# Optimization experiments

Measured on AMD Instinct MI355X. Metric: run time of the kernel, lower is better.

The kernel has to match this reference:

```python
import jax, jax.numpy as jnp
import numpy as np

EMBED, HEADS, LEVELS, POINTS = 256, 8, 4, 4
SPATIAL_SHAPES = np.array([[128, 128], [64, 64], [32, 32], [16, 16]], dtype=np.int32)


def _grid_init_bias():
    # Faithful reproduction of the sampling_offsets bias init (per-head directional grid).
    thetas = np.arange(HEADS, dtype=np.float32) * (2.0 * np.pi / HEADS)
    g = np.stack([np.cos(thetas), np.sin(thetas)], -1)
    g = g / np.abs(g).max(-1, keepdims=True)
    g = np.tile(g.reshape(HEADS, 1, 1, 2), (1, LEVELS, POINTS, 1))
    for i in range(POINTS):
        g[:, :, i, :] *= i + 1
    return g.reshape(-1).astype(np.float32)


def setup_inputs() -> dict:
    key = jax.random.key(0)
    ks = jax.random.split(key, 8)
    bs = 2
    V = int((SPATIAL_SHAPES[:, 0] * SPATIAL_SHAPES[:, 1]).sum())  # 21760
    Q = V  # encoder self-attention
    C = EMBED
    n_off = HEADS * LEVELS * POINTS * 2
    n_attn = HEADS * LEVELS * POINTS
    inv_sqrt_c = 1.0 / np.sqrt(C)
    return {
        "query": jax.random.normal(ks[0], (bs, Q, C), jnp.float32),
        "value": jax.random.normal(ks[1], (bs, V, C), jnp.float32),
        "reference_points": jax.random.uniform(ks[2], (bs, Q, LEVELS, 2), jnp.float32),
        "spatial_shapes": SPATIAL_SHAPES,  # static int array
        # learned parameters (torch Linear stored as [in, out]: y = x @ W + b)
        "W_off": jax.random.normal(ks[3], (C, n_off), jnp.float32) * 0.01,
        "b_off": jnp.asarray(_grid_init_bias()),
        "W_attn": jax.random.normal(ks[4], (C, n_attn), jnp.float32) * 0.02,
        "b_attn": jnp.zeros((n_attn,), jnp.float32),
        "W_v": jax.random.normal(ks[5], (C, C), jnp.float32) * inv_sqrt_c,
        "b_v": jnp.zeros((C,), jnp.float32),
        "W_out": jax.random.normal(ks[6], (C, C), jnp.float32) * inv_sqrt_c,
        "b_out": jnp.zeros((C,), jnp.float32),
    }


def _ms_deform_attn(query, value, reference_points, shapes,
                    W_off, b_off, W_attn, b_attn, W_v, b_v, W_out, b_out):
    bs, Q, C = query.shape
    d = C // HEADS
    # value projection -> [bs, heads, V, d]
    val = (value @ W_v + b_v).reshape(bs, -1, HEADS, d).transpose(0, 2, 1, 3)
    # sampling offsets and attention weights from query
    off = (query @ W_off + b_off).reshape(bs, Q, HEADS, LEVELS, POINTS, 2)
    attn = jax.nn.softmax(
        (query @ W_attn + b_attn).reshape(bs, Q, HEADS, LEVELS * POINTS), axis=-1
    ).reshape(bs, Q, HEADS, LEVELS, POINTS)
    # offset normalizer is (W, H) per level
    norm = jnp.asarray(np.stack([shapes[:, 1], shapes[:, 0]], -1), jnp.float32)  # [L,2]
    loc = reference_points[:, :, None, :, None, :] + off / norm[None, None, None, :, None, :]

    out = jnp.zeros((bs, HEADS, Q, d), query.dtype)
    start = 0
    for l in range(LEVELS):
        H, W = int(shapes[l, 0]), int(shapes[l, 1])
        v_l = val[:, :, start:start + H * W]  # [bs, heads, H*W, d]
        start += H * W
        loc_l = loc[:, :, :, l]    # [bs, Q, heads, P, 2] in [0,1]
        attn_l = attn[:, :, :, l]  # [bs, Q, heads, P]
        # grid_sample(align_corners=False, padding_mode='zeros') semantics
        g = 2.0 * loc_l - 1.0
        x = (g[..., 0] + 1.0) * 0.5 * W - 0.5
        y = (g[..., 1] + 1.0) * 0.5 * H - 0.5
        x0 = jnp.floor(x)
        y0 = jnp.floor(y)
        for dx in (0, 1):
            for dy in (0, 1):
                xi = x0 + dx
                yi = y0 + dy
                w = (1.0 - jnp.abs(x - xi)) * (1.0 - jnp.abs(y - yi))
                valid = (xi >= 0) & (xi <= W - 1) & (yi >= 0) & (yi <= H - 1)
                w = jnp.where(valid, w, 0.0) * attn_l  # fused corner + attention weight
                idx = (jnp.clip(yi, 0, H - 1).astype(jnp.int32) * W
                       + jnp.clip(xi, 0, W - 1).astype(jnp.int32))  # [bs,Q,heads,P]
                idx_t = jnp.transpose(idx, (0, 2, 1, 3)).reshape(bs, HEADS, Q * POINTS)
                vals = jnp.take_along_axis(v_l, idx_t[..., None], axis=2)
                vals = vals.reshape(bs, HEADS, Q, POINTS, d)
                out = out + jnp.einsum('bhqpd,bqhp->bhqd', vals, w)
    out = out.transpose(0, 2, 1, 3).reshape(bs, Q, C)  # heads-major channel layout
    return out @ W_out + b_out


def reference(query, value, reference_points, spatial_shapes,
              W_off, b_off, W_attn, b_attn, W_v, b_v, W_out, b_out):
    shapes = np.asarray(spatial_shapes)  # static
    return _ms_deform_attn(query, value, reference_points, shapes,
                           W_off, b_off, W_attn, b_attn, W_v, b_v, W_out, b_out)
```

## Files before the change

kernel.cpp:

```cpp
#include <hip/hip_runtime.h>
#include <math.h>

#define QN 21760
#define MTOT 43520
#define SZBQC 11141120

typedef __attribute__((ext_vector_type(8))) short bf16x8;
typedef __attribute__((ext_vector_type(4))) float f32x4;

__device__ inline ushort f2bf(float f) {
  union { float f; uint u; } v; v.f = f;
  return (ushort)((v.u + 0x7FFFu + ((v.u >> 16) & 1u)) >> 16);
}
__device__ inline uint pk2(float lo, float hi) { return (uint)f2bf(lo) | ((uint)f2bf(hi) << 16); }

__device__ inline void g2l(const ushort* g, ushort* l) {
  __builtin_amdgcn_global_load_lds(
      (const __attribute__((address_space(1))) void*)g,
      (__attribute__((address_space(3))) void*)l, 16, 0, 0);
}

__global__ __launch_bounds__(256) void prep_weights(
    const float* __restrict__ Wv, const float* __restrict__ Wout,
    const float* __restrict__ Woff, const float* __restrict__ Wattn,
    const float* __restrict__ boff, const float* __restrict__ battn,
    ushort* __restrict__ wv_t, ushort* __restrict__ wout_t,
    ushort* __restrict__ wol_t, float* __restrict__ biasf) {
  int bidx = blockIdx.x, t = threadIdx.x;
  if (bidx < 256) {
    int idx = bidx * 256 + t; int n = idx >> 8, k = idx & 255;
    wv_t[idx] = f2bf(Wv[(size_t)k * 256 + n]);
  } else if (bidx < 512) {
    int idx = (bidx - 256) * 256 + t; int n = idx >> 8, k = idx & 255;
    wout_t[idx] = f2bf(Wout[(size_t)k * 256 + n]);
  } else {
    int idx = (bidx - 512) * 256 + t; int n = idx >> 8, k = idx & 255;
    float v = (n < 256) ? Woff[(size_t)k * 256 + n] : Wattn[(size_t)k * 128 + (n - 256)];
    wol_t[idx] = f2bf(v);
    if (idx < 384) biasf[idx] = (idx < 256) ? boff[idx] : battn[idx - 256];
  }
}


__global__ __launch_bounds__(256) void gemm_in(
    const float* __restrict__ value, const float* __restrict__ query,
    const ushort* __restrict__ Wv, const ushort* __restrict__ Wol,
    const float* __restrict__ bv, const float* __restrict__ bol,
    ushort* __restrict__ val_out, float* __restrict__ offlog) {
  __shared__ ushort As[2][4096];
  __shared__ ushort Bs[2][4096];
  const int t = threadIdx.x, wave = t >> 6, lane = t & 63;
  const int bx = blockIdx.y, bm = blockIdx.x * 128;
  const bool isVal = bx < 2;
  const float* A   = isVal ? value : query;
  const ushort* Bt = isVal ? (Wv + (size_t)bx * 128 * 256)
                           : (Wol + (size_t)(bx - 2) * 128 * 256);
  const int wm = (wave >> 1) * 64, wn = (wave & 1) * 64;
  const int l15 = lane & 15, l4 = lane >> 4;
  const int pc = l4 ^ ((l15 >> 1) & 3);

  const int srow = lane >> 2;
  const int sch  = (lane & 3) ^ ((lane >> 3) & 3);
  const ushort* Bg = Bt + (size_t)(32 * wave + srow) * 256 + sch * 8;
  ushort* lb[2] = { &Bs[0][(32 * wave) * 32], &Bs[1][(32 * wave) * 32] };

  f32x4 acc[4][4];
#pragma unroll
  for (int i = 0; i < 4; ++i)
#pragma unroll
    for (int j = 0; j < 4; ++j) acc[i][j] = (f32x4){0.f, 0.f, 0.f, 0.f};

  int arow[4], apart[4];
#pragma unroll
  for (int i = 0; i < 4; ++i) {
    int c = t + i * 256; arow[i] = c >> 3; apart[i] = c & 7;
  }

  {
    float4 pa[4];
#pragma unroll
    for (int i = 0; i < 4; ++i)
      pa[i] = *(const float4*)&A[(size_t)(bm + arow[i]) * 256 + apart[i] * 4];
    g2l(Bg, lb[0]); g2l(Bg + 16 * 256, lb[0] + 16 * 32);
#pragma unroll
    for (int i = 0; i < 4; ++i) {
      int pc16 = (apart[i] >> 1) ^ ((arow[i] >> 1) & 3);
      ushort4 hv = { f2bf(pa[i].x), f2bf(pa[i].y), f2bf(pa[i].z), f2bf(pa[i].w) };
      *(ushort4*)&As[0][arow[i] * 32 + pc16 * 8 + (apart[i] & 1) * 4] = hv;
    }
  }

  for (int k = 0; k < 8; ++k) {
    __syncthreads();
    const int cur = k & 1, nxt = cur ^ 1;
    float4 pa[4];
    if (k < 7) {
      int k1 = (k + 1) * 32;
#pragma unroll
      for (int i = 0; i < 4; ++i)
        pa[i] = *(const float4*)&A[(size_t)(bm + arow[i]) * 256 + k1 + apart[i] * 4];
      g2l(Bg + k1, lb[nxt]); g2l(Bg + 16 * 256 + k1, lb[nxt] + 16 * 32);
    }
    bf16x8 af[4], bfr[4];
#pragma unroll
    for (int mi = 0; mi < 4; ++mi)
      af[mi] = *(const bf16x8*)&As[cur][(wm + mi * 16 + l15) * 32 + pc * 8];
#pragma unroll
    for (int ni = 0; ni < 4; ++ni)
      bfr[ni] = *(const bf16x8*)&Bs[cur][(wn + ni * 16 + l15) * 32 + pc * 8];
#pragma unroll
    for (int mi = 0; mi < 4; ++mi)
#pragma unroll
      for (int ni = 0; ni < 4; ++ni)
        acc[mi][ni] = __builtin_amdgcn_mfma_f32_16x16x32_bf16(af[mi], bfr[ni], acc[mi][ni], 0, 0, 0);
    if (k < 7) {
#pragma unroll
      for (int i = 0; i < 4; ++i) {
        int pc16 = (apart[i] >> 1) ^ ((arow[i] >> 1) & 3);
        ushort4 hv = { f2bf(pa[i].x), f2bf(pa[i].y), f2bf(pa[i].z), f2bf(pa[i].w) };
        *(ushort4*)&As[nxt][arow[i] * 32 + pc16 * 8 + (apart[i] & 1) * 4] = hv;
      }
    }
  }

  if (isVal) {
    _Float16* vo = (_Float16*)val_out;
#pragma unroll
    for (int mi = 0; mi < 4; ++mi)
#pragma unroll
      for (int ni = 0; ni < 4; ++ni) {
        int col = bx * 128 + wn + ni * 16 + l15;
        float bb = bv[col];
        int hh = col >> 5, c = col & 31;
#pragma unroll
        for (int r = 0; r < 4; ++r) {
          int row = bm + wm + mi * 16 + l4 * 4 + r;
          int b = (row >= QN) ? 1 : 0;
          int vpos = row - b * QN;
          vo[((size_t)(b * 8 + hh) * QN + vpos) * 32 + c] = (_Float16)(acc[mi][ni][r] + bb);
        }
      }
  } else {
#pragma unroll
    for (int mi = 0; mi < 4; ++mi)
#pragma unroll
      for (int ni = 0; ni < 4; ++ni) {
        int col = (bx - 2) * 128 + wn + ni * 16 + l15;
        float bb = bol[col];
#pragma unroll
        for (int r = 0; r < 4; ++r) {
          int row = bm + wm + mi * 16 + l4 * 4 + r;
          offlog[(size_t)row * 384 + col] = acc[mi][ni][r] + bb;
        }
      }
  }
}

__global__ __launch_bounds__(256) void gemm_out(
    const ushort* __restrict__ A, const ushort* __restrict__ Bt,
    const float* __restrict__ bias, float* __restrict__ C) {
  __shared__ ushort As[2][4096];
  __shared__ ushort Bs[2][4096];
  const int t = threadIdx.x, wave = t >> 6, lane = t & 63;
  const int bm = blockIdx.x * 128, bn = blockIdx.y * 128;
  const int wm = (wave >> 1) * 64, wn = (wave & 1) * 64;
  const int l15 = lane & 15, l4 = lane >> 4;
  const int pc = l4 ^ ((l15 >> 1) & 3);

  const int srow = lane >> 2;
  const int sch  = (lane & 3) ^ ((lane >> 3) & 3);
  const ushort* Ag = A + (size_t)(bm + 32 * wave + srow) * 256 + sch * 8;
  const ushort* Bg = Bt + (size_t)(bn + 32 * wave + srow) * 256 + sch * 8;
  ushort* la[2] = { &As[0][(32 * wave) * 32], &As[1][(32 * wave) * 32] };
  ushort* lb[2] = { &Bs[0][(32 * wave) * 32], &Bs[1][(32 * wave) * 32] };

  f32x4 acc[4][4];
#pragma unroll
  for (int i = 0; i < 4; ++i)
#pragma unroll
    for (int j = 0; j < 4; ++j) acc[i][j] = (f32x4){0.f, 0.f, 0.f, 0.f};

  g2l(Ag, la[0]); g2l(Ag + 16 * 256, la[0] + 16 * 32);
  g2l(Bg, lb[0]); g2l(Bg + 16 * 256, lb[0] + 16 * 32);

  for (int k = 0; k < 8; ++k) {
    __syncthreads();
    const int cur = k & 1, nxt = cur ^ 1;
    if (k < 7) {
      int k1 = (k + 1) * 32;
      g2l(Ag + k1, la[nxt]); g2l(Ag + 16 * 256 + k1, la[nxt] + 16 * 32);
      g2l(Bg + k1, lb[nxt]); g2l(Bg + 16 * 256 + k1, lb[nxt] + 16 * 32);
    }
    bf16x8 af[4], bfr[4];
#pragma unroll
    for (int mi = 0; mi < 4; ++mi)
      af[mi] = *(const bf16x8*)&As[cur][(wm + mi * 16 + l15) * 32 + pc * 8];
#pragma unroll
    for (int ni = 0; ni < 4; ++ni)
      bfr[ni] = *(const bf16x8*)&Bs[cur][(wn + ni * 16 + l15) * 32 + pc * 8];
#pragma unroll
    for (int mi = 0; mi < 4; ++mi)
#pragma unroll
      for (int ni = 0; ni < 4; ++ni)
        acc[mi][ni] = __builtin_amdgcn_mfma_f32_16x16x32_bf16(af[mi], bfr[ni], acc[mi][ni], 0, 0, 0);
  }

#pragma unroll
  for (int mi = 0; mi < 4; ++mi)
#pragma unroll
    for (int ni = 0; ni < 4; ++ni) {
      int col = bn + wn + ni * 16 + l15;
      float bb = bias[col];
#pragma unroll
      for (int r = 0; r < 4; ++r) {
        int row = bm + wm + mi * 16 + l4 * 4 + r;
        C[(size_t)row * 256 + col] = acc[mi][ni][r] + bb;
      }
    }
}

__device__ inline void fmah(float* a, uint4 u, float wv) {
  union { uint4 u; _Float16 h[8]; } c; c.u = u;
#pragma unroll
  for (int i = 0; i < 8; ++i) a[i] = fmaf((float)c.h[i], wv, a[i]);
}

__global__ __launch_bounds__(256) void msda_sample(
    const ushort* __restrict__ val, const float* __restrict__ offlog,
    const float* __restrict__ ref, ushort* __restrict__ interm) {
  const int lsz[4]    = {128, 64, 32, 16};
  const int lstart[4] = {0, 16384, 20480, 21504};

  int h   = blockIdx.x & 7;
  int z   = blockIdx.x >> 3;
  int sub = threadIdx.x & 3;
  int bq  = z * 64 + (threadIdx.x >> 2);
  int b   = (bq >= QN) ? 1 : 0;

  const float* lgp = offlog + (size_t)bq * 384 + 256 + h * 16;
  float w[16];
  {
    float4 a0 = *(const float4*)(lgp);
    float4 a1 = *(const float4*)(lgp + 4);
    float4 a2 = *(const float4*)(lgp + 8);
    float4 a3 = *(const float4*)(lgp + 12);
    w[0]=a0.x; w[1]=a0.y; w[2]=a0.z; w[3]=a0.w;
    w[4]=a1.x; w[5]=a1.y; w[6]=a1.z; w[7]=a1.w;
    w[8]=a2.x; w[9]=a2.y; w[10]=a2.z; w[11]=a2.w;
    w[12]=a3.x; w[13]=a3.y; w[14]=a3.z; w[15]=a3.w;
  }
  float m = -1e30f;
#pragma unroll
  for (int s = 0; s < 16; ++s) m = fmaxf(m, w[s]);
  float sum = 0.f;
#pragma unroll
  for (int s = 0; s < 16; ++s) { w[s] = __expf(w[s] - m); sum += w[s]; }
  float inv = 1.f / sum;

  const float* offp = offlog + (size_t)bq * 384 + h * 32;
  const float* refp = ref + (size_t)bq * 8;
  const ushort* vb  = val + ((size_t)(b * 8 + h) * QN) * 32 + sub * 8;

  float acc[8];
#pragma unroll
  for (int i = 0; i < 8; ++i) acc[i] = 0.f;

#pragma unroll
  for (int l = 0; l < 4; ++l) {
    float4 o0 = *(const float4*)(offp + l * 8);
    float4 o1 = *(const float4*)(offp + l * 8 + 4);
    float ox[4] = { o0.x, o0.z, o1.x, o1.z };
    float oy[4] = { o0.y, o0.w, o1.y, o1.w };
    const int   W = lsz[l];
    const float fW = (float)W;
    const int   base = lstart[l];
    const float rx = refp[l * 2 + 0], ry = refp[l * 2 + 1];
#pragma unroll
    for (int p = 0; p < 4; ++p) {
      float x = rx * fW + ox[p] - 0.5f;
      float y = ry * fW + oy[p] - 0.5f;
      float x0f = floorf(x), y0f = floorf(y);
      int   x0 = (int)x0f,   y0 = (int)y0f;
      float fx = x - x0f,    fy = y - y0f;
      float a = w[l * 4 + p] * inv;
      const ushort* r0 = vb + (size_t)(base + y0 * W + x0) * 32;
      const ushort* r1 = r0 + (size_t)W * 32;

      if (x0 >= 0 && y0 >= 0 && x0 + 1 < W && y0 + 1 < W) {
        uint4 u00 = *(const uint4*)r0;
        uint4 u10 = *(const uint4*)(r0 + 32);
        uint4 u01 = *(const uint4*)r1;
        uint4 u11 = *(const uint4*)(r1 + 32);
        float w00 = (1.f - fx) * (1.f - fy) * a;
        float w10 = fx * (1.f - fy) * a;
        float w01 = (1.f - fx) * fy * a;
        float w11 = fx * fy * a;
        fmah(acc, u00, w00); fmah(acc, u10, w10);
        fmah(acc, u01, w01); fmah(acc, u11, w11);
      } else {
        float wx0 = (x0 >= 0 && x0 < W) ? (1.f - fx) : 0.f;
        float wx1 = (x0 + 1 >= 0 && x0 + 1 < W) ? fx : 0.f;
        float wy0 = (y0 >= 0 && y0 < W) ? (1.f - fy) : 0.f;
        float wy1 = (y0 + 1 >= 0 && y0 + 1 < W) ? fy : 0.f;
        float w00 = wx0 * wy0 * a, w10 = wx1 * wy0 * a;
        float w01 = wx0 * wy1 * a, w11 = wx1 * wy1 * a;
        if (w00 != 0.f) { uint4 u = *(const uint4*)r0;        fmah(acc, u, w00); }
        if (w10 != 0.f) { uint4 u = *(const uint4*)(r0 + 32); fmah(acc, u, w10); }
        if (w01 != 0.f) { uint4 u = *(const uint4*)r1;        fmah(acc, u, w01); }
        if (w11 != 0.f) { uint4 u = *(const uint4*)(r1 + 32); fmah(acc, u, w11); }
      }
    }
  }

  uint4 o;
  o.x = pk2(acc[0], acc[1]); o.y = pk2(acc[2], acc[3]);
  o.z = pk2(acc[4], acc[5]); o.w = pk2(acc[6], acc[7]);
  *(uint4*)(interm + (size_t)bq * 256 + h * 32 + sub * 8) = o;
}

extern "C" void kernel_launch(void* const* d_in, const int* in_sizes, int n_in,
                              void* d_out, int out_size, void* d_ws, size_t ws_size,
                              hipStream_t stream) {
  const float* query = (const float*)d_in[0];
  const float* value = (const float*)d_in[1];
  const float* ref   = (const float*)d_in[2];
  const float* W_off  = (const float*)d_in[4];
  const float* b_off  = (const float*)d_in[5];
  const float* W_attn = (const float*)d_in[6];
  const float* b_attn = (const float*)d_in[7];
  const float* W_v    = (const float*)d_in[8];
  const float* b_v    = (const float*)d_in[9];
  const float* W_out  = (const float*)d_in[10];
  const float* b_out  = (const float*)d_in[11];
  float* out = (float*)d_out;

  char* wsb = (char*)d_ws;
  ushort* ws_wv     = (ushort*)(wsb + 0);
  ushort* ws_wol    = (ushort*)(wsb + 131072);
  ushort* ws_wout   = (ushort*)(wsb + 327680);
  float*  ws_biasf  = (float*)(wsb + 458752);
  ushort* ws_val    = (ushort*)(wsb + 462848);
  ushort* ws_interm = (ushort*)(wsb + 22745088);
  float*  ws_offlog = (float*)(wsb + 45027328);
  size_t need = (size_t)45027328 + 66846720;
  if (ws_size < need) return;

  dim3 blk(256);
  prep_weights<<<dim3(896), blk, 0, stream>>>(W_v, W_out, W_off, W_attn, b_off, b_attn,
                                              ws_wv, ws_wout, ws_wol, ws_biasf);
  gemm_in<<<dim3(340, 5), blk, 0, stream>>>(value, query, ws_wv, ws_wol, b_v, ws_biasf,
                                            ws_val, ws_offlog);
  msda_sample<<<dim3(5440), blk, 0, stream>>>(ws_val, ws_offlog, ref, ws_interm);
  gemm_out<<<dim3(340, 2), blk, 0, stream>>>(ws_interm, ws_wout, b_out, out);
}
```

Measured before the change: 286.6 us.

## Keep full-K A tile resident in LDS and sweep all N panels per block

New measurement: 290.4 us. About the same (+1.3%).

```diff
diff --git a/kernel.cpp b/kernel.cpp
--- a/kernel.cpp
+++ b/kernel.cpp
@@ -3,7 +3,6 @@
 
 #define QN 21760
 #define MTOT 43520
-#define SZBQC 11141120
 
 typedef __attribute__((ext_vector_type(8))) short bf16x8;
 typedef __attribute__((ext_vector_type(4))) float f32x4;
@@ -42,181 +41,186 @@
 }
 
 
-__global__ __launch_bounds__(256) void gemm_in(
+__global__ __launch_bounds__(256) void gemm_in2(
     const float* __restrict__ value, const float* __restrict__ query,
     const ushort* __restrict__ Wv, const ushort* __restrict__ Wol,
     const float* __restrict__ bv, const float* __restrict__ bol,
     ushort* __restrict__ val_out, float* __restrict__ offlog) {
-  __shared__ ushort As[2][4096];
+  __shared__ ushort Ares[8 * 2048];
   __shared__ ushort Bs[2][4096];
   const int t = threadIdx.x, wave = t >> 6, lane = t & 63;
-  const int bx = blockIdx.y, bm = blockIdx.x * 128;
-  const bool isVal = bx < 2;
-  const float* A   = isVal ? value : query;
-  const ushort* Bt = isVal ? (Wv + (size_t)bx * 128 * 256)
-                           : (Wol + (size_t)(bx - 2) * 128 * 256);
-  const int wm = (wave >> 1) * 64, wn = (wave & 1) * 64;
+  const int bm = blockIdx.x * 64;
+  const bool isVal = (blockIdx.y == 0);
+  const float* A    = isVal ? value : query;
+  const ushort* Bt0 = isVal ? Wv : Wol;
+  const int np = isVal ? 2 : 3;
   const int l15 = lane & 15, l4 = lane >> 4;
   const int pc = l4 ^ ((l15 >> 1) & 3);
-
-  const int srow = lane >> 2;
-  const int sch  = (lane & 3) ^ ((lane >> 3) & 3);
-  const ushort* Bg = Bt + (size_t)(32 * wave + srow) * 256 + sch * 8;
+  const int wm = (wave >> 1) * 32, wn = (wave & 1) * 64;
+
+  const float4* Af4 = (const float4*)(A + (size_t)bm * 256);
+#pragma unroll
+  for (int i = 0; i < 16; ++i) {
+    int f = i * 256 + t;
+    int row = f >> 6, col4 = f & 63;
+    float4 v = Af4[f];
+    int k = col4 >> 3, part = col4 & 7;
+    int pc16 = (part >> 1) ^ ((row >> 1) & 3);
+    ushort4 hv = { f2bf(v.x), f2bf(v.y), f2bf(v.z), f2bf(v.w) };
+    *(ushort4*)&Ares[k * 2048 + row * 32 + pc16 * 8 + (part & 1) * 4] = hv;
+  }
+
+  const int srow = lane >> 2, sch = (lane & 3) ^ ((lane >> 3) & 3);
+  const int brow = 32 * wave + srow;
   ushort* lb[2] = { &Bs[0][(32 * wave) * 32], &Bs[1][(32 * wave) * 32] };
-
-  f32x4 acc[4][4];
-#pragma unroll
-  for (int i = 0; i < 4; ++i)
+  {
+    const ushort* Bg = Bt0 + (size_t)brow * 256 + sch * 8;
+    g2l(Bg, lb[0]); g2l(Bg + 16 * 256, lb[0] + 16 * 32);
+  }
+
+  f32x4 acc[2][4];
+#pragma unroll
+  for (int i = 0; i < 2; ++i)
 #pragma unroll
     for (int j = 0; j < 4; ++j) acc[i][j] = (f32x4){0.f, 0.f, 0.f, 0.f};
 
-  int arow[4], apart[4];
-#pragma unroll
-  for (int i = 0; i < 4; ++i) {
-    int c = t + i * 256; arow[i] = c >> 3; apart[i] = c & 7;
-  }
-
-  {
-    float4 pa[4];
-#pragma unroll
-    for (int i = 0; i < 4; ++i)
-      pa[i] = *(const float4*)&A[(size_t)(bm + arow[i]) * 256 + apart[i] * 4];
-    g2l(Bg, lb[0]); g2l(Bg + 16 * 256, lb[0] + 16 * 32);
-#pragma unroll
-    for (int i = 0; i < 4; ++i) {
-      int pc16 = (apart[i] >> 1) ^ ((arow[i] >> 1) & 3);
-      ushort4 hv = { f2bf(pa[i].x), f2bf(pa[i].y), f2bf(pa[i].z), f2bf(pa[i].w) };
-      *(ushort4*)&As[0][arow[i] * 32 + pc16 * 8 + (apart[i] & 1) * 4] = hv;
-    }
-  }
-
-  for (int k = 0; k < 8; ++k) {
+  const int total = np * 8;
+  for (int j = 0; j < total; ++j) {
     __syncthreads();
-    const int cur = k & 1, nxt = cur ^ 1;
-    float4 pa[4];
-    if (k < 7) {
-      int k1 = (k + 1) * 32;
-#pragma unroll
-      for (int i = 0; i < 4; ++i)
-        pa[i] = *(const float4*)&A[(size_t)(bm + arow[i]) * 256 + k1 + apart[i] * 4];
-      g2l(Bg + k1, lb[nxt]); g2l(Bg + 16 * 256 + k1, lb[nxt] + 16 * 32);
-    }
-    bf16x8 af[4], bfr[4];
-#pragma unroll
-    for (int mi = 0; mi < 4; ++mi)
-      af[mi] = *(const bf16x8*)&As[cur][(wm + mi * 16 + l15) * 32 + pc * 8];
+    const int cur = j & 1, nxt = cur ^ 1;
+    if (j + 1 < total) {
+      int jn = j + 1, pn = jn >> 3, kn = jn & 7;
+      const ushort* Bg = Bt0 + (size_t)(pn * 128 + brow) * 256 + kn * 32 + sch * 8;
+      g2l(Bg, lb[nxt]); g2l(Bg + 16 * 256, lb[nxt] + 16 * 32);
+    }
+    const int k = j & 7;
+    bf16x8 af[2], bfr[4];
+#pragma unroll
+    for (int mi = 0; mi < 2; ++mi)
+      af[mi] = *(const bf16x8*)&Ares[k * 2048 + (wm + mi * 16 + l15) * 32 + pc * 8];
 #pragma unroll
     for (int ni = 0; ni < 4; ++ni)
       bfr[ni] = *(const bf16x8*)&Bs[cur][(wn + ni * 16 + l15) * 32 + pc * 8];
 #pragma unroll
-    for (int mi = 0; mi < 4; ++mi)
+    for (int mi = 0; mi < 2; ++mi)
 #pragma unroll
       for (int ni = 0; ni < 4; ++ni)
         acc[mi][ni] = __builtin_amdgcn_mfma_f32_16x16x32_bf16(af[mi], bfr[ni], acc[mi][ni], 0, 0, 0);
-    if (k < 7) {
-#pragma unroll
-      for (int i = 0; i < 4; ++i) {
-        int pc16 = (apart[i] >> 1) ^ ((arow[i] >> 1) & 3);
-        ushort4 hv = { f2bf(pa[i].x), f2bf(pa[i].y), f2bf(pa[i].z), f2bf(pa[i].w) };
-        *(ushort4*)&As[nxt][arow[i] * 32 + pc16 * 8 + (apart[i] & 1) * 4] = hv;
+
+    if (k == 7) {
+      const int p = j >> 3;
+      if (isVal) {
+        _Float16* vo = (_Float16*)val_out;
+#pragma unroll
+        for (int mi = 0; mi < 2; ++mi)
+#pragma unroll
+          for (int ni = 0; ni < 4; ++ni) {
+            int col = p * 128 + wn + ni * 16 + l15;
+            float bb = bv[col];
+            int hh = col >> 5, c = col & 31;
+#pragma unroll
+            for (int r = 0; r < 4; ++r) {
+              int row = bm + wm + mi * 16 + l4 * 4 + r;
+              int b = (row >= QN) ? 1 : 0;
+              int vpos = row - b * QN;
+              vo[((size_t)(b * 8 + hh) * QN + vpos) * 32 + c] = (_Float16)(acc[mi][ni][r] + bb);
+            }
+          }
+      } else {
+#pragma unroll
+        for (int mi = 0; mi < 2; ++mi)
+#pragma unroll
+          for (int ni = 0; ni < 4; ++ni) {
+            int col = p * 128 + wn + ni * 16 + l15;
+            float bb = bol[col];
+#pragma unroll
+            for (int r = 0; r < 4; ++r) {
+              int row = bm + wm + mi * 16 + l4 * 4 + r;
+              offlog[(size_t)row * 384 + col] = acc[mi][ni][r] + bb;
+            }
+          }
       }
-    }
-  }
-
-  if (isVal) {
-    _Float16* vo = (_Float16*)val_out;
-#pragma unroll
-    for (int mi = 0; mi < 4; ++mi)
-#pragma unroll
-      for (int ni = 0; ni < 4; ++ni) {
-        int col = bx * 128 + wn + ni * 16 + l15;
-        float bb = bv[col];
-        int hh = col >> 5, c = col & 31;
-#pragma unroll
-        for (int r = 0; r < 4; ++r) {
-          int row = bm + wm + mi * 16 + l4 * 4 + r;
-          int b = (row >= QN) ? 1 : 0;
-          int vpos = row - b * QN;
-          vo[((size_t)(b * 8 + hh) * QN + vpos) * 32 + c] = (_Float16)(acc[mi][ni][r] + bb);
-        }
-      }
-  } else {
-#pragma unroll
-    for (int mi = 0; mi < 4; ++mi)
-#pragma unroll
-      for (int ni = 0; ni < 4; ++ni) {
-        int col = (bx - 2) * 128 + wn + ni * 16 + l15;
-        float bb = bol[col];
-#pragma unroll
-        for (int r = 0; r < 4; ++r) {
-          int row = bm + wm + mi * 16 + l4 * 4 + r;
-          offlog[(size_t)row * 384 + col] = acc[mi][ni][r] + bb;
-        }
-      }
-  }
-}
-
-__global__ __launch_bounds__(256) void gemm_out(
+#pragma unroll
+      for (int i = 0; i < 2; ++i)
+#pragma unroll
+        for (int jj = 0; jj < 4; ++jj) acc[i][jj] = (f32x4){0.f, 0.f, 0.f, 0.f};
+    }
+  }
+}
+
+__global__ __launch_bounds__(256) void gemm_out2(
     const ushort* __restrict__ A, const ushort* __restrict__ Bt,
     const float* __restrict__ bias, float* __restrict__ C) {
-  __shared__ ushort As[2][4096];
+  __shared__ ushort Ares[8 * 2048];
   __shared__ ushort Bs[2][4096];
   const int t = threadIdx.x, wave = t >> 6, lane = t & 63;
-  const int bm = blockIdx.x * 128, bn = blockIdx.y * 128;
-  const int wm = (wave >> 1) * 64, wn = (wave & 1) * 64;
+  const int bm = blockIdx.x * 64;
   const int l15 = lane & 15, l4 = lane >> 4;
   const int pc = l4 ^ ((l15 >> 1) & 3);
-
-  const int srow = lane >> 2;
-  const int sch  = (lane & 3) ^ ((lane >> 3) & 3);
-  const ushort* Ag = A + (size_t)(bm + 32 * wave + srow) * 256 + sch * 8;
-  const ushort* Bg = Bt + (size_t)(bn + 32 * wave + srow) * 256 + sch * 8;
-  ushort* la[2] = { &As[0][(32 * wave) * 32], &As[1][(32 * wave) * 32] };
+  const int wm = (wave >> 1) * 32, wn = (wave & 1) * 64;
+  const int srow = lane >> 2, sch = (lane & 3) ^ ((lane >> 3) & 3);
+
+  const int rowbase = 16 * wave;
+  const ushort* Ag = A + (size_t)(bm + rowbase + srow) * 256 + sch * 8;
+#pragma unroll
+  for (int k = 0; k < 8; ++k)
+    g2l(Ag + k * 32, &Ares[k * 2048 + rowbase * 32]);
+
+  const int brow = 32 * wave + srow;
   ushort* lb[2] = { &Bs[0][(32 * wave) * 32], &Bs[1][(32 * wave) * 32] };
-
-  f32x4 acc[4][4];
-#pragma unroll
-  for (int i = 0; i < 4; ++i)
+  {
+    const ushort* Bg = Bt + (size_t)brow * 256 + sch * 8;
+    g2l(Bg, lb[0]); g2l(Bg + 16 * 256, lb[0] + 16 * 32);
+  }
+
+  f32x4 acc[2][4];
+#pragma unroll
+  for (int i = 0; i < 2; ++i)
 #pragma unroll
     for (int j = 0; j < 4; ++j) acc[i][j] = (f32x4){0.f, 0.f, 0.f, 0.f};
 
-  g2l(Ag, la[0]); g2l(Ag + 16 * 256, la[0] + 16 * 32);
-  g2l(Bg, lb[0]); g2l(Bg + 16 * 256, lb[0] + 16 * 32);
-
-  for (int k = 0; k < 8; ++k) {
+  for (int j = 0; j < 16; ++j) {
     __syncthreads();
-    const int cur = k & 1, nxt = cur ^ 1;
-    if (k < 7) {
-      int k1 = (k + 1) * 32;
-      g2l(Ag + k1, la[nxt]); g2l(Ag + 16 * 256 + k1, la[nxt] + 16 * 32);
-      g2l(Bg + k1, lb[nxt]); g2l(Bg + 16 * 256 + k1, lb[nxt] + 16 * 32);
-    }
-    bf16x8 af[4], bfr[4];
-#pragma unroll
-    for (int mi = 0; mi < 4; ++mi)
-      af[mi] = *(const bf16x8*)&As[cur][(wm + mi * 16 + l15) * 32 + pc * 8];
+    const int cur = j & 1, nxt = cur ^ 1;
+    if (j + 1 < 16) {
+      int jn = j + 1, pn = jn >> 3, kn = jn & 7;
+      const ushort* Bg = Bt + (size_t)(pn * 128 + brow) * 256 + kn * 32 + sch * 8;
+      g2l(Bg, lb[nxt]); g2l(Bg + 16 * 256, lb[nxt] + 16 * 32);
+    }
+    const int k = j & 7;
+    bf16x8 af[2], bfr[4];
+#pragma unroll
+    for (int mi = 0; mi < 2; ++mi)
+      af[mi] = *(const bf16x8*)&Ares[k * 2048 + (wm + mi * 16 + l15) * 32 + pc * 8];
 #pragma unroll
     for (int ni = 0; ni < 4; ++ni)
       bfr[ni] = *(const bf16x8*)&Bs[cur][(wn + ni * 16 + l15) * 32 + pc * 8];
 #pragma unroll
-    for (int mi = 0; mi < 4; ++mi)
+    for (int mi = 0; mi < 2; ++mi)
 #pragma unroll
       for (int ni = 0; ni < 4; ++ni)
         acc[mi][ni] = __builtin_amdgcn_mfma_f32_16x16x32_bf16(af[mi], bfr[ni], acc[mi][ni], 0, 0, 0);
-  }
-
-#pragma unroll
-  for (int mi = 0; mi < 4; ++mi)
-#pragma unroll
-    for (int ni = 0; ni < 4; ++ni) {
-      int col = bn + wn + ni * 16 + l15;
-      float bb = bias[col];
-#pragma unroll
-      for (int r = 0; r < 4; ++r) {
-        int row = bm + wm + mi * 16 + l4 * 4 + r;
-        C[(size_t)row * 256 + col] = acc[mi][ni][r] + bb;
-      }
-    }
+
+    if (k == 7) {
+      const int p = j >> 3;
+#pragma unroll
+      for (int mi = 0; mi < 2; ++mi)
+#pragma unroll
+        for (int ni = 0; ni < 4; ++ni) {
+          int col = p * 128 + wn + ni * 16 + l15;
+          float bb = bias[col];
+#pragma unroll
+          for (int r = 0; r < 4; ++r) {
+            int row = bm + wm + mi * 16 + l4 * 4 + r;
+            C[(size_t)row * 256 + col] = acc[mi][ni][r] + bb;
+          }
+        }
+#pragma unroll
+      for (int i = 0; i < 2; ++i)
+#pragma unroll
+        for (int jj = 0; jj < 4; ++jj) acc[i][jj] = (f32x4){0.f, 0.f, 0.f, 0.f};
+    }
+  }
 }
 
 __device__ inline void fmah(float* a, uint4 u, float wv) {
@@ -348,8 +352,8 @@
   dim3 blk(256);
   prep_weights<<<dim3(896), blk, 0, stream>>>(W_v, W_out, W_off, W_attn, b_off, b_attn,
                                               ws_wv, ws_wout, ws_wol, ws_biasf);
-  gemm_in<<<dim3(340, 5), blk, 0, stream>>>(value, query, ws_wv, ws_wol, b_v, ws_biasf,
-                                            ws_val, ws_offlog);
+  gemm_in2<<<dim3(680, 2), blk, 0, stream>>>(value, query, ws_wv, ws_wol, b_v, ws_biasf,
+                                             ws_val, ws_offlog);
   msda_sample<<<dim3(5440), blk, 0, stream>>>(ws_val, ws_offlog, ref, ws_interm);
-  gemm_out<<<dim3(340, 2), blk, 0, stream>>>(ws_interm, ws_wout, b_out, out);
-}
+  gemm_out2<<<dim3(680), blk, 0, stream>>>(ws_interm, ws_wout, b_out, out);
+}
```
